# Performance work log

Measured on AMD Instinct MI355X. Metric: run time of the kernel, lower is better.

## Reference

```python
import jax, jax.numpy as jnp
import numpy as np

N_NODES = 100000
N_EDGES = 1600000
D = 128


def setup_inputs() -> dict:
    key = jax.random.key(0)
    k1, k2, k3, k4, k5 = jax.random.split(key, 5)
    scale = 1.0 / np.sqrt(D)
    return {
        "x": jax.random.normal(k1, (N_NODES, D), dtype=jnp.float32),
        "edge_index": jax.random.randint(k2, (2, N_EDGES), 0, N_NODES, dtype=jnp.int64),
        "edge_attr": jax.random.normal(k3, (N_EDGES, D), dtype=jnp.float32),
        "w1": jax.random.normal(k4, (D, D), dtype=jnp.float32) * scale,
        "b1": jnp.zeros((D,), dtype=jnp.float32),
        "w2": jax.random.normal(k5, (D, D), dtype=jnp.float32) * scale,
        "b2": jnp.zeros((D,), dtype=jnp.float32),
    }


def reference(x, edge_index, edge_attr, w1, b1, w2, b2):
    # GINEConv: out = MLP((1+eps)*x + sum_{j->i} ReLU(x_j + e_ij)), eps=0
    src = edge_index[0]  # source node j per edge
    dst = edge_index[1]  # target node i per edge
    msg = jax.nn.relu(x[src] + edge_attr)            # [E, D] edge-wise gather + relu
    agg = jax.ops.segment_sum(msg, dst, num_segments=N_NODES)  # [N, D] scatter-sum
    h = x + agg                                      # (1 + eps)*x with eps = 0
    h = jax.nn.relu(h @ w1 + b1)                     # Linear -> ReLU
    return h @ w2 + b2                               # Linear
```

## Files before the change

### kernel.cpp

```cpp
#include <hip/hip_runtime.h>
#include <stdint.h>

#define N_NODES 100000
#define N_EDGES 1600000
#define D 128
#define ROWS_PAD 100096

typedef long long i64;
typedef __attribute__((ext_vector_type(8))) short bf16x8;
typedef __attribute__((ext_vector_type(4))) float f32x4;
typedef __attribute__((ext_vector_type(4))) float fv4;
typedef __attribute__((ext_vector_type(4))) unsigned short usv4;
typedef __attribute__((ext_vector_type(8))) unsigned short usv8;

__device__ __forceinline__ unsigned short f2bf(float f) {
    union { float f; unsigned u; } v; v.f = f;
    unsigned r = v.u + 0x7fff + ((v.u >> 16) & 1);
    return (unsigned short)(r >> 16);
}
__device__ __forceinline__ float bf2f(unsigned short h) {
    union { unsigned u; float f; } v; v.u = ((unsigned)h) << 16;
    return v.f;
}

__global__ __launch_bounds__(256) void xcvt_kernel(
    const float* __restrict__ x, unsigned short* __restrict__ xb)
{
    const i64 b = ((i64)blockIdx.x * 256 + threadIdx.x) * 8;
    if (b < (i64)N_NODES * D) {
        const fv4 u0 = *reinterpret_cast<const fv4*>(x + b);
        const fv4 u1 = *reinterpret_cast<const fv4*>(x + b + 4);
        usv8 o;
        o.s0 = f2bf(u0.x); o.s1 = f2bf(u0.y); o.s2 = f2bf(u0.z); o.s3 = f2bf(u0.w);
        o.s4 = f2bf(u1.x); o.s5 = f2bf(u1.y); o.s6 = f2bf(u1.z); o.s7 = f2bf(u1.w);
        *reinterpret_cast<usv8*>(xb + b) = o;
    }
}

#define SCAN_CHUNK 1024
#define SCAN_THREADS 256
#define N_CHUNKS ((N_NODES + SCAN_CHUNK - 1) / SCAN_CHUNK)

__global__ __launch_bounds__(256) void count_zero_kernel(int* __restrict__ counts)
{
    const int i = blockIdx.x * 256 + threadIdx.x;
    if (i < N_NODES) counts[i] = 0;
}

__global__ __launch_bounds__(256) void hist_kernel(
    const int* __restrict__ dst, int* __restrict__ counts)
{
    const int e = blockIdx.x * 256 + threadIdx.x;
    if (e < N_EDGES) atomicAdd(&counts[dst[e]], 1);
}

__global__ __launch_bounds__(SCAN_THREADS) void scan_pass1(
    const int* __restrict__ counts, int* __restrict__ blockSums)
{
    __shared__ int sdata[SCAN_THREADS];
    const int b = blockIdx.x, t = threadIdx.x;
    const int base = b * SCAN_CHUNK + t * 4;
    int s = 0;
    #pragma unroll
    for (int k = 0; k < 4; ++k) {
        const int i = base + k;
        if (i < N_NODES) s += counts[i];
    }
    sdata[t] = s; __syncthreads();
    for (int off = SCAN_THREADS / 2; off > 0; off >>= 1) {
        if (t < off) sdata[t] += sdata[t + off];
        __syncthreads();
    }
    if (t == 0) blockSums[b] = sdata[0];
}

__global__ __launch_bounds__(128) void scan_pass2(
    int* __restrict__ blockSums, int* __restrict__ offsets)
{
    __shared__ int sh[128];
    const int t = threadIdx.x;
    const int v = (t < N_CHUNKS) ? blockSums[t] : 0;
    sh[t] = v; __syncthreads();
    for (int off = 1; off < 128; off <<= 1) {
        const int add = (t >= off) ? sh[t - off] : 0;
        __syncthreads();
        sh[t] += add;
        __syncthreads();
    }
    const int incl = sh[t];
    if (t < N_CHUNKS) blockSums[t] = incl - v;
    if (t == N_CHUNKS - 1) offsets[N_NODES] = incl;
}

__global__ __launch_bounds__(SCAN_THREADS) void scan_pass3(
    const int* __restrict__ counts, const int* __restrict__ blockSums,
    int* __restrict__ offsets, int* __restrict__ cursor)
{
    __shared__ int sh[SCAN_THREADS];
    const int b = blockIdx.x, t = threadIdx.x;
    const int base = b * SCAN_CHUNK + t * 4;
    int v[4]; int s = 0;
    #pragma unroll
    for (int k = 0; k < 4; ++k) {
        const int i = base + k;
        v[k] = (i < N_NODES) ? counts[i] : 0;
        s += v[k];
    }
    sh[t] = s; __syncthreads();
    for (int off = 1; off < SCAN_THREADS; off <<= 1) {
        const int add = (t >= off) ? sh[t - off] : 0;
        __syncthreads();
        sh[t] += add;
        __syncthreads();
    }
    int run = blockSums[b] + (sh[t] - s);
    #pragma unroll
    for (int k = 0; k < 4; ++k) {
        const int i = base + k;
        if (i < N_NODES) { offsets[i] = run; cursor[i] = run; }
        run += v[k];
    }
}

__global__ __launch_bounds__(256) void fill_kernel(
    const int* __restrict__ dst, int* __restrict__ cursor, int* __restrict__ bucket)
{
    const int e = blockIdx.x * 256 + threadIdx.x;
    if (e < N_EDGES) {
        const int pos = atomicAdd(&cursor[dst[e]], 1);
        bucket[pos] = e;
    }
}

__global__ __launch_bounds__(256) void pad_zero_kernel(
    unsigned short* __restrict__ h0, unsigned short* __restrict__ h1)
{
    const int i = blockIdx.x * 256 + threadIdx.x;
    const int PADE = (ROWS_PAD - N_NODES) * D;
    if (i < PADE) {
        h0[(i64)N_NODES * D + i] = 0;
        h1[(i64)N_NODES * D + i] = 0;
    }
}

#define PAIR(p) {                                                               \
    const int idx = 2*(p) + half;                                               \
    const bool v = idx < n;                                                     \
    int e_ = __shfl(key, idx);                                                  \
    int s_ = __shfl(sk, idx);                                                   \
    e_ = v ? e_ : 0; s_ = v ? s_ : 0;                                           \
    const usv4 xv = *reinterpret_cast<const usv4*>(xb + (i64)s_ * D + c4);      \
    const fv4 ev = __builtin_nontemporal_load(                                  \
        reinterpret_cast<const fv4*>(ea + (i64)e_ * D + c4));                   \
    if (v) {                                                                    \
        acc.x += fmaxf(bf2f(xv.x) + ev.x, 0.f);                                 \
        acc.y += fmaxf(bf2f(xv.y) + ev.y, 0.f);                                 \
        acc.z += fmaxf(bf2f(xv.z) + ev.z, 0.f);                                 \
        acc.w += fmaxf(bf2f(xv.w) + ev.w, 0.f);                                 \
    }                                                                           \
}

__global__ __launch_bounds__(256) void gather_kernel(
    const float* __restrict__ x,
    const unsigned short* __restrict__ xb,
    const int*   __restrict__ srcIdx,
    const float* __restrict__ ea,
    const int*   __restrict__ offsets,
    const int*   __restrict__ bucket,
    unsigned short* __restrict__ h0)
{
    const int wave = threadIdx.x >> 6;
    const int lane = threadIdx.x & 63;
    const int node = blockIdx.x * 4 + wave;
    if (node >= N_NODES) return;
    const int half = lane >> 5;
    const int c4   = (lane & 31) * 4;

    const int p0 = offsets[node];
    const int p1 = offsets[node + 1];

    fv4 acc;
    if (half == 0) acc = *reinterpret_cast<const fv4*>(x + (i64)node * D + c4);
    else           acc = (fv4){0.f, 0.f, 0.f, 0.f};

    for (int base = p0; base < p1; base += 64) {
        const int n = min(64, p1 - base);

        int key = 0x7fffffff;
        if (lane < n) key = bucket[base + lane];

        #pragma unroll
        for (int k = 2; k <= 64; k <<= 1) {
            #pragma unroll
            for (int j = k >> 1; j > 0; j >>= 1) {
                const int other = __shfl_xor(key, j);
                const bool up    = ((lane & k) == 0);
                const bool lower = ((lane & j) == 0);
                key = (lower == up) ? min(key, other) : max(key, other);
            }
        }

        int sk = 0;
        if (lane < n) sk = srcIdx[key];

        const int npair = (n + 1) >> 1;
        int it = 0;
        for (; it + 3 < npair; it += 4) {
            PAIR(it) PAIR(it + 1) PAIR(it + 2) PAIR(it + 3)
        }
        for (; it < npair; ++it) { PAIR(it) }
    }

    acc.x += __shfl_xor(acc.x, 32);
    acc.y += __shfl_xor(acc.y, 32);
    acc.z += __shfl_xor(acc.z, 32);
    acc.w += __shfl_xor(acc.w, 32);

    if (half == 0) {
        usv4 o;
        o.x = f2bf(acc.x); o.y = f2bf(acc.y);
        o.z = f2bf(acc.z); o.w = f2bf(acc.w);
        *reinterpret_cast<usv4*>(h0 + (i64)node * D + c4) = o;
    }
}

__global__ __launch_bounds__(256) void mlp1_mfma_kernel(
    const unsigned short* __restrict__ hin,
    const float* __restrict__ w,
    const float* __restrict__ bias,
    unsigned short* __restrict__ hout)
{
    const int tid  = threadIdx.x;
    const int wave = tid >> 6;
    const int lane = tid & 63;
    const int g    = lane >> 4;
    const int lr   = lane & 15;
    const int colbase = wave * 32;

    bf16x8 bfrag[4][2];
    #pragma unroll
    for (int ks = 0; ks < 4; ++ks) {
        #pragma unroll
        for (int nt = 0; nt < 2; ++nt) {
            const int col = colbase + nt * 16 + lr;
            const int k0  = ks * 32 + g * 8;
            bf16x8 f;
            #pragma unroll
            for (int j = 0; j < 8; ++j)
                f[j] = (short)f2bf(w[(k0 + j) * D + col]);
            bfrag[ks][nt] = f;
        }
    }
    const float bc0 = bias[colbase + lr];
    const float bc1 = bias[colbase + 16 + lr];

    const int rowbase0 = blockIdx.x * 128;
    #pragma unroll 1
    for (int sub = 0; sub < 8; ++sub) {
        const int rowbase = rowbase0 + sub * 16;
        const int arow = rowbase + lr;

        bf16x8 afrag[4];
        #pragma unroll
        for (int ks = 0; ks < 4; ++ks)
            afrag[ks] = *reinterpret_cast<const bf16x8*>(
                hin + (i64)arow * D + ks * 32 + g * 8);

        f32x4 acc0 = { bc0, bc0, bc0, bc0 };
        f32x4 acc1 = { bc1, bc1, bc1, bc1 };
        #pragma unroll
        for (int ks = 0; ks < 4; ++ks) {
            acc0 = __builtin_amdgcn_mfma_f32_16x16x32_bf16(afrag[ks], bfrag[ks][0], acc0, 0, 0, 0);
            acc1 = __builtin_amdgcn_mfma_f32_16x16x32_bf16(afrag[ks], bfrag[ks][1], acc1, 0, 0, 0);
        }

        #pragma unroll
        for (int r = 0; r < 4; ++r) {
            const int orow = rowbase + g * 4 + r;
            hout[(i64)orow * D + colbase + lr]      = f2bf(fmaxf(acc0[r], 0.f));
            hout[(i64)orow * D + colbase + 16 + lr] = f2bf(fmaxf(acc1[r], 0.f));
        }
    }
}

__global__ __launch_bounds__(256) void mlp2_mfma_kernel(
    const unsigned short* __restrict__ hin,
    const float* __restrict__ w,
    const float* __restrict__ bias,
    float* __restrict__ hout)
{
    const int tid  = threadIdx.x;
    const int wave = tid >> 6;
    const int lane = tid & 63;
    const int g    = lane >> 4;
    const int lr   = lane & 15;
    const int colbase = wave * 32;

    bf16x8 bfrag[4][2];
    #pragma unroll
    for (int ks = 0; ks < 4; ++ks) {
        #pragma unroll
        for (int nt = 0; nt < 2; ++nt) {
            const int col = colbase + nt * 16 + lr;
            const int k0  = ks * 32 + g * 8;
            bf16x8 f;
            #pragma unroll
            for (int j = 0; j < 8; ++j)
                f[j] = (short)f2bf(w[(k0 + j) * D + col]);
            bfrag[ks][nt] = f;
        }
    }
    const float bc0 = bias[colbase + lr];
    const float bc1 = bias[colbase + 16 + lr];

    const int rowbase0 = blockIdx.x * 128;
    #pragma unroll 1
    for (int sub = 0; sub < 8; ++sub) {
        const int rowbase = rowbase0 + sub * 16;
        const int arow = rowbase + lr;

        bf16x8 afrag[4];
        #pragma unroll
        for (int ks = 0; ks < 4; ++ks)
            afrag[ks] = *reinterpret_cast<const bf16x8*>(
                hin + (i64)arow * D + ks * 32 + g * 8);

        f32x4 acc0 = { bc0, bc0, bc0, bc0 };
        f32x4 acc1 = { bc1, bc1, bc1, bc1 };
        #pragma unroll
        for (int ks = 0; ks < 4; ++ks) {
            acc0 = __builtin_amdgcn_mfma_f32_16x16x32_bf16(afrag[ks], bfrag[ks][0], acc0, 0, 0, 0);
            acc1 = __builtin_amdgcn_mfma_f32_16x16x32_bf16(afrag[ks], bfrag[ks][1], acc1, 0, 0, 0);
        }

        #pragma unroll
        for (int r = 0; r < 4; ++r) {
            const int orow = rowbase + g * 4 + r;
            if (orow < N_NODES) {
                hout[(i64)orow * D + colbase + lr]      = acc0[r];
                hout[(i64)orow * D + colbase + 16 + lr] = acc1[r];
            }
        }
    }
}

__global__ __launch_bounds__(256) void init_acc_kernel(
    const float* __restrict__ x, float* __restrict__ acc)
{
    const int i = blockIdx.x * blockDim.x + threadIdx.x;
    const int n = N_NODES * D / 4;
    if (i < n)
        reinterpret_cast<float4*>(acc)[i] = reinterpret_cast<const float4*>(x)[i];
}

__global__ __launch_bounds__(256) void edge_scatter_kernel(
    const float* __restrict__ x,
    const int*  __restrict__ src,
    const int*  __restrict__ dst,
    const float* __restrict__ ea,
    float* __restrict__ acc)
{
    const int lane = threadIdx.x & 31;
    const int grp  = threadIdx.x >> 5;
    const i64 e = (i64)blockIdx.x * 8 + grp;
    if (e >= N_EDGES) return;
    const int s = src[e];
    const int d = dst[e];
    const int j = lane * 4;
    const float4 xv = *reinterpret_cast<const float4*>(x  + (i64)s * D + j);
    const float4 ev = *reinterpret_cast<const float4*>(ea + e * D + j);
    float4 m;
    m.x = fmaxf(xv.x + ev.x, 0.0f);
    m.y = fmaxf(xv.y + ev.y, 0.0f);
    m.z = fmaxf(xv.z + ev.z, 0.0f);
    m.w = fmaxf(xv.w + ev.w, 0.0f);
    float* pp = acc + (i64)d * D + j;
    atomicAdd(pp + 0, m.x);
    atomicAdd(pp + 1, m.y);
    atomicAdd(pp + 2, m.z);
    atomicAdd(pp + 3, m.w);
}

#define MLP_THREADS 512
#define ROWS_PER_CHUNK 16
#define CHUNKS_PER_BLOCK 4
#define ROWS_PER_BLOCK (ROWS_PER_CHUNK * CHUNKS_PER_BLOCK)

template<bool RELU>
__global__ __launch_bounds__(MLP_THREADS) void mlp_layer_kernel(
    const float* __restrict__ hin,
    const float* __restrict__ w,
    const float* __restrict__ b,
    float* __restrict__ hout)
{
    __shared__ float ws_[D * D];
    __shared__ float bs_[D];
    __shared__ float hrow[ROWS_PER_CHUNK][D];

    const int tid = threadIdx.x;
    for (int t = tid; t < D * D / 4; t += MLP_THREADS)
        reinterpret_cast<float4*>(ws_)[t] = reinterpret_cast<const float4*>(w)[t];
    if (tid < D) bs_[tid] = b[tid];

    const int j = tid & (D - 1);
    const int q = tid >> 7;
    const int rowBase = blockIdx.x * ROWS_PER_BLOCK;

    for (int c = 0; c < CHUNKS_PER_BLOCK; ++c) {
        const int chunkRow = rowBase + c * ROWS_PER_CHUNK;
        __syncthreads();
        {
            const int r   = tid >> 5;
            const int col = (tid & 31) * 4;
            const int gi  = chunkRow + r;
            float4 v = make_float4(0.f, 0.f, 0.f, 0.f);
            if (gi < N_NODES)
                v = *reinterpret_cast<const float4*>(hin + (i64)gi * D + col);
            *reinterpret_cast<float4*>(&hrow[r][col]) = v;
        }
        __syncthreads();

        float acc0 = bs_[j], acc1 = bs_[j], acc2 = bs_[j], acc3 = bs_[j];
        const int r0 = q * 4;
        #pragma unroll 4
        for (int k = 0; k < D; ++k) {
            const float wv = ws_[k * D + j];
            acc0 = fmaf(hrow[r0 + 0][k], wv, acc0);
            acc1 = fmaf(hrow[r0 + 1][k], wv, acc1);
            acc2 = fmaf(hrow[r0 + 2][k], wv, acc2);
            acc3 = fmaf(hrow[r0 + 3][k], wv, acc3);
        }
        if (RELU) {
            acc0 = fmaxf(acc0, 0.f); acc1 = fmaxf(acc1, 0.f);
            acc2 = fmaxf(acc2, 0.f); acc3 = fmaxf(acc3, 0.f);
        }
        const int gi = chunkRow + r0;
        if (gi + 0 < N_NODES) hout[(i64)(gi + 0) * D + j] = acc0;
        if (gi + 1 < N_NODES) hout[(i64)(gi + 1) * D + j] = acc1;
        if (gi + 2 < N_NODES) hout[(i64)(gi + 2) * D + j] = acc2;
        if (gi + 3 < N_NODES) hout[(i64)(gi + 3) * D + j] = acc3;
    }
}

extern "C" void kernel_launch(void* const* d_in, const int* in_sizes, int n_in,
                              void* d_out, int out_size, void* d_ws, size_t ws_size,
                              hipStream_t stream)
{
    const float* x  = (const float*)d_in[0];
    const int*   ei = (const int*)  d_in[1];
    const float* ea = (const float*)d_in[2];
    const float* w1 = (const float*)d_in[3];
    const float* b1 = (const float*)d_in[4];
    const float* w2 = (const float*)d_in[5];
    const float* b2 = (const float*)d_in[6];
    float* out = (float*)d_out;

    const int* src = ei;
    const int* dst = ei + N_EDGES;

    const size_t INT_REGION = (size_t)N_NODES + (N_NODES + 1) + N_NODES + 128 + N_EDGES;
    const size_t X_ELEMS    = (size_t)N_NODES * D;
    const size_t H_ELEMS    = (size_t)ROWS_PAD * D;
    const size_t WS_NEEDED  = INT_REGION * 4 + 64 + (X_ELEMS + 2 * H_ELEMS) * 2;

    if (ws_size >= WS_NEEDED) {
        int* counts    = (int*)d_ws;
        int* offsets   = counts + N_NODES;
        int* cursor    = offsets + (N_NODES + 1);
        int* blockSums = cursor + N_NODES;
        int* bucket    = blockSums + 128;
        uintptr_t p = (uintptr_t)(bucket + N_EDGES);
        p = (p + 63) & ~(uintptr_t)63;
        unsigned short* xb = (unsigned short*)p;
        unsigned short* h0 = xb + X_ELEMS;
        unsigned short* h1 = h0 + H_ELEMS;

        xcvt_kernel<<<(int)(X_ELEMS / 8 + 255) / 256, 256, 0, stream>>>(x, xb);
        count_zero_kernel<<<(N_NODES + 255) / 256, 256, 0, stream>>>(counts);
        hist_kernel<<<(N_EDGES + 255) / 256, 256, 0, stream>>>(dst, counts);
        scan_pass1<<<N_CHUNKS, SCAN_THREADS, 0, stream>>>(counts, blockSums);
        scan_pass2<<<1, 128, 0, stream>>>(blockSums, offsets);
        scan_pass3<<<N_CHUNKS, SCAN_THREADS, 0, stream>>>(counts, blockSums, offsets, cursor);
        fill_kernel<<<(N_EDGES + 255) / 256, 256, 0, stream>>>(dst, cursor, bucket);
        pad_zero_kernel<<<48, 256, 0, stream>>>(h0, h1);
        gather_kernel<<<(N_NODES + 3) / 4, 256, 0, stream>>>(x, xb, src, ea, offsets, bucket, h0);

        const int mlpBlocks = ROWS_PAD / 128;
        mlp1_mfma_kernel<<<mlpBlocks, 256, 0, stream>>>(h0, w1, b1, h1);
        mlp2_mfma_kernel<<<mlpBlocks, 256, 0, stream>>>(h1, w2, b2, out);
    } else {
        const int n = N_NODES * D / 4;
        init_acc_kernel<<<(n + 255) / 256, 256, 0, stream>>>(x, out);
        edge_scatter_kernel<<<(N_EDGES + 7) / 8, 256, 0, stream>>>(x, src, dst, ea, out);
        const int blocks = (N_NODES + ROWS_PER_BLOCK - 1) / ROWS_PER_BLOCK;
        mlp_layer_kernel<true ><<<blocks, MLP_THREADS, 0, stream>>>(out, w1, b1, out);
        mlp_layer_kernel<false><<<blocks, MLP_THREADS, 0, stream>>>(out, w2, b2, out);
    }
}
```

Measured before the change: 486.7 us.

## Fuse MLP layers via LDS, pack src into bucket, merge prep kernels

Fuses the two MLP MFMA kernels into one that keeps the hidden layer in shared memory rather than writing and rereading it from global memory. The fill kernel now stores (edge, src) pairs so the gather kernel no longer does a dependent srcIdx lookup; both values are carried through the bitonic sort. The bf16 conversion, count zeroing and pad zeroing are merged into one prep kernel, which removes launches. The self term now comes from the bf16 copy of x instead of fp32 x, which slightly lowers precision.

```diff
diff --git a/kernel.cpp b/kernel.cpp
--- a/kernel.cpp
+++ b/kernel.cpp
@@ -23,10 +23,12 @@
     return v.f;
 }
 
-__global__ __launch_bounds__(256) void xcvt_kernel(
-    const float* __restrict__ x, unsigned short* __restrict__ xb)
-{
-    const i64 b = ((i64)blockIdx.x * 256 + threadIdx.x) * 8;
+__global__ __launch_bounds__(256) void prep_kernel(
+    const float* __restrict__ x, unsigned short* __restrict__ xb,
+    int* __restrict__ counts, unsigned short* __restrict__ h0)
+{
+    const int i = blockIdx.x * 256 + threadIdx.x;
+    const i64 b = (i64)i * 8;
     if (b < (i64)N_NODES * D) {
         const fv4 u0 = *reinterpret_cast<const fv4*>(x + b);
         const fv4 u1 = *reinterpret_cast<const fv4*>(x + b + 4);
@@ -35,17 +37,14 @@
         o.s4 = f2bf(u1.x); o.s5 = f2bf(u1.y); o.s6 = f2bf(u1.z); o.s7 = f2bf(u1.w);
         *reinterpret_cast<usv8*>(xb + b) = o;
     }
+    if (i < N_NODES) counts[i] = 0;
+    if (i < (ROWS_PAD - N_NODES) * D)
+        h0[(i64)N_NODES * D + i] = 0;
 }
 
 #define SCAN_CHUNK 1024
 #define SCAN_THREADS 256
 #define N_CHUNKS ((N_NODES + SCAN_CHUNK - 1) / SCAN_CHUNK)
-
-__global__ __launch_bounds__(256) void count_zero_kernel(int* __restrict__ counts)
-{
-    const int i = blockIdx.x * 256 + threadIdx.x;
-    if (i < N_NODES) counts[i] = 0;
-}
 
 __global__ __launch_bounds__(256) void hist_kernel(
     const int* __restrict__ dst, int* __restrict__ counts)
@@ -122,24 +121,14 @@
     }
 }
 
-__global__ __launch_bounds__(256) void fill_kernel(
-    const int* __restrict__ dst, int* __restrict__ cursor, int* __restrict__ bucket)
+__global__ __launch_bounds__(256) void fill2_kernel(
+    const int* __restrict__ src, const int* __restrict__ dst,
+    int* __restrict__ cursor, int2* __restrict__ bucket2)
 {
     const int e = blockIdx.x * 256 + threadIdx.x;
     if (e < N_EDGES) {
         const int pos = atomicAdd(&cursor[dst[e]], 1);
-        bucket[pos] = e;
-    }
-}
-
-__global__ __launch_bounds__(256) void pad_zero_kernel(
-    unsigned short* __restrict__ h0, unsigned short* __restrict__ h1)
-{
-    const int i = blockIdx.x * 256 + threadIdx.x;
-    const int PADE = (ROWS_PAD - N_NODES) * D;
-    if (i < PADE) {
-        h0[(i64)N_NODES * D + i] = 0;
-        h1[(i64)N_NODES * D + i] = 0;
+        bucket2[pos] = make_int2(e, src[e]);
     }
 }
 
@@ -147,7 +136,7 @@
     const int idx = 2*(p) + half;                                               \
     const bool v = idx < n;                                                     \
     int e_ = __shfl(key, idx);                                                  \
-    int s_ = __shfl(sk, idx);                                                   \
+    int s_ = __shfl(sv, idx);                                                   \
     e_ = v ? e_ : 0; s_ = v ? s_ : 0;                                           \
     const usv4 xv = *reinterpret_cast<const usv4*>(xb + (i64)s_ * D + c4);      \
     const fv4 ev = __builtin_nontemporal_load(                                  \
@@ -161,12 +150,10 @@
 }
 
 __global__ __launch_bounds__(256) void gather_kernel(
-    const float* __restrict__ x,
     const unsigned short* __restrict__ xb,
-    const int*   __restrict__ srcIdx,
     const float* __restrict__ ea,
-    const int*   __restrict__ offsets,
-    const int*   __restrict__ bucket,
+    const int*  __restrict__ offsets,
+    const int2* __restrict__ bucket2,
     unsigned short* __restrict__ h0)
 {
     const int wave = threadIdx.x >> 6;
@@ -179,29 +166,34 @@
     const int p0 = offsets[node];
     const int p1 = offsets[node + 1];
 
-    fv4 acc;
-    if (half == 0) acc = *reinterpret_cast<const fv4*>(x + (i64)node * D + c4);
-    else           acc = (fv4){0.f, 0.f, 0.f, 0.f};
+    fv4 acc = (fv4){0.f, 0.f, 0.f, 0.f};
+    if (half == 0) {
+        const usv4 xv = *reinterpret_cast<const usv4*>(xb + (i64)node * D + c4);
+        acc.x = bf2f(xv.x); acc.y = bf2f(xv.y);
+        acc.z = bf2f(xv.z); acc.w = bf2f(xv.w);
+    }
 
     for (int base = p0; base < p1; base += 64) {
         const int n = min(64, p1 - base);
 
-        int key = 0x7fffffff;
-        if (lane < n) key = bucket[base + lane];
+        int key = 0x7fffffff, sv = 0;
+        if (lane < n) {
+            const int2 t = bucket2[base + lane];
+            key = t.x; sv = t.y;
+        }
 
         #pragma unroll
         for (int k = 2; k <= 64; k <<= 1) {
             #pragma unroll
             for (int j = k >> 1; j > 0; j >>= 1) {
-                const int other = __shfl_xor(key, j);
+                const int ok = __shfl_xor(key, j);
+                const int os = __shfl_xor(sv, j);
                 const bool up    = ((lane & k) == 0);
                 const bool lower = ((lane & j) == 0);
-                key = (lower == up) ? min(key, other) : max(key, other);
+                const bool take  = (lower == up) ? (ok < key) : (ok > key);
+                if (take) { key = ok; sv = os; }
             }
         }
-
-        int sk = 0;
-        if (lane < n) sk = srcIdx[key];
 
         const int npair = (n + 1) >> 1;
         int it = 0;
@@ -224,18 +216,21 @@
     }
 }
 
-__global__ __launch_bounds__(256) void mlp1_mfma_kernel(
+__global__ __launch_bounds__(256) void mlp_fused_kernel(
     const unsigned short* __restrict__ hin,
-    const float* __restrict__ w,
-    const float* __restrict__ bias,
-    unsigned short* __restrict__ hout)
-{
+    const float* __restrict__ w1, const float* __restrict__ b1,
+    const float* __restrict__ w2, const float* __restrict__ b2,
+    float* __restrict__ out)
+{
+    __shared__ unsigned short h1[128][136];
+
     const int tid  = threadIdx.x;
     const int wave = tid >> 6;
     const int lane = tid & 63;
     const int g    = lane >> 4;
     const int lr   = lane & 15;
     const int colbase = wave * 32;
+    const int rowbase0 = blockIdx.x * 128;
 
     bf16x8 bfrag[4][2];
     #pragma unroll
@@ -247,18 +242,16 @@
             bf16x8 f;
             #pragma unroll
             for (int j = 0; j < 8; ++j)
-                f[j] = (short)f2bf(w[(k0 + j) * D + col]);
+                f[j] = (short)f2bf(w1[(k0 + j) * D + col]);
             bfrag[ks][nt] = f;
         }
     }
-    const float bc0 = bias[colbase + lr];
-    const float bc1 = bias[colbase + 16 + lr];
-
-    const int rowbase0 = blockIdx.x * 128;
+    float bc0 = b1[colbase + lr];
+    float bc1 = b1[colbase + 16 + lr];
+
     #pragma unroll 1
     for (int sub = 0; sub < 8; ++sub) {
-        const int rowbase = rowbase0 + sub * 16;
-        const int arow = rowbase + lr;
+        const int arow = rowbase0 + sub * 16 + lr;
 
         bf16x8 afrag[4];
         #pragma unroll
@@ -276,27 +269,14 @@
 
         #pragma unroll
         for (int r = 0; r < 4; ++r) {
-            const int orow = rowbase + g * 4 + r;
-            hout[(i64)orow * D + colbase + lr]      = f2bf(fmaxf(acc0[r], 0.f));
-            hout[(i64)orow * D + colbase + 16 + lr] = f2bf(fmaxf(acc1[r], 0.f));
-        }
-    }
-}
-
-__global__ __launch_bounds__(256) void mlp2_mfma_kernel(
-    const unsigned short* __restrict__ hin,
-    const float* __restrict__ w,
-    const float* __restrict__ bias,
-    float* __restrict__ hout)
-{
-    const int tid  = threadIdx.x;
-    const int wave = tid >> 6;
-    const int lane = tid & 63;
-    const int g    = lane >> 4;
-    const int lr   = lane & 15;
-    const int colbase = wave * 32;
-
-    bf16x8 bfrag[4][2];
+            const int rl = sub * 16 + g * 4 + r;
+            h1[rl][colbase + lr]      = f2bf(fmaxf(acc0[r], 0.f));
+            h1[rl][colbase + 16 + lr] = f2bf(fmaxf(acc1[r], 0.f));
+        }
+    }
+
+    __syncthreads();
+
     #pragma unroll
     for (int ks = 0; ks < 4; ++ks) {
         #pragma unroll
@@ -306,24 +286,21 @@
             bf16x8 f;
             #pragma unroll
             for (int j = 0; j < 8; ++j)
-                f[j] = (short)f2bf(w[(k0 + j) * D + col]);
+                f[j] = (short)f2bf(w2[(k0 + j) * D + col]);
             bfrag[ks][nt] = f;
         }
     }
-    const float bc0 = bias[colbase + lr];
-    const float bc1 = bias[colbase + 16 + lr];
-
-    const int rowbase0 = blockIdx.x * 128;
+    bc0 = b2[colbase + lr];
+    bc1 = b2[colbase + 16 + lr];
+
     #pragma unroll 1
     for (int sub = 0; sub < 8; ++sub) {
-        const int rowbase = rowbase0 + sub * 16;
-        const int arow = rowbase + lr;
+        const int rl = sub * 16 + lr;
 
         bf16x8 afrag[4];
         #pragma unroll
         for (int ks = 0; ks < 4; ++ks)
-            afrag[ks] = *reinterpret_cast<const bf16x8*>(
-                hin + (i64)arow * D + ks * 32 + g * 8);
+            afrag[ks] = *reinterpret_cast<const bf16x8*>(&h1[rl][ks * 32 + g * 8]);
 
         f32x4 acc0 = { bc0, bc0, bc0, bc0 };
         f32x4 acc1 = { bc1, bc1, bc1, bc1 };
@@ -335,10 +312,10 @@
 
         #pragma unroll
         for (int r = 0; r < 4; ++r) {
-            const int orow = rowbase + g * 4 + r;
+            const int orow = rowbase0 + sub * 16 + g * 4 + r;
             if (orow < N_NODES) {
-                hout[(i64)orow * D + colbase + lr]      = acc0[r];
-                hout[(i64)orow * D + colbase + 16 + lr] = acc1[r];
+                out[(i64)orow * D + colbase + lr]      = acc0[r];
+                out[(i64)orow * D + colbase + 16 + lr] = acc1[r];
             }
         }
     }
@@ -458,36 +435,33 @@
     const int* src = ei;
     const int* dst = ei + N_EDGES;
 
-    const size_t INT_REGION = (size_t)N_NODES + (N_NODES + 1) + N_NODES + 128 + N_EDGES;
+    const size_t INT_REGION = (size_t)N_NODES + (N_NODES + 1) + N_NODES + 128;
     const size_t X_ELEMS    = (size_t)N_NODES * D;
     const size_t H_ELEMS    = (size_t)ROWS_PAD * D;
-    const size_t WS_NEEDED  = INT_REGION * 4 + 64 + (X_ELEMS + 2 * H_ELEMS) * 2;
+    const size_t WS_NEEDED  = INT_REGION * 4 + 64 + (size_t)N_EDGES * 8 + 64
+                            + (X_ELEMS + H_ELEMS) * 2;
 
     if (ws_size >= WS_NEEDED) {
         int* counts    = (int*)d_ws;
         int* offsets   = counts + N_NODES;
         int* cursor    = offsets + (N_NODES + 1);
         int* blockSums = cursor + N_NODES;
-        int* bucket    = blockSums + 128;
-        uintptr_t p = (uintptr_t)(bucket + N_EDGES);
+        uintptr_t p = (uintptr_t)(blockSums + 128);
+        p = (p + 63) & ~(uintptr_t)63;
+        int2* bucket2 = (int2*)p;
+        p = (uintptr_t)(bucket2 + N_EDGES);
         p = (p + 63) & ~(uintptr_t)63;
         unsigned short* xb = (unsigned short*)p;
         unsigned short* h0 = xb + X_ELEMS;
-        unsigned short* h1 = h0 + H_ELEMS;
-
-        xcvt_kernel<<<(int)(X_ELEMS / 8 + 255) / 256, 256, 0, stream>>>(x, xb);
-        count_zero_kernel<<<(N_NODES + 255) / 256, 256, 0, stream>>>(counts);
+
+        prep_kernel<<<(int)(X_ELEMS / 8 + 255) / 256, 256, 0, stream>>>(x, xb, counts, h0);
         hist_kernel<<<(N_EDGES + 255) / 256, 256, 0, stream>>>(dst, counts);
         scan_pass1<<<N_CHUNKS, SCAN_THREADS, 0, stream>>>(counts, blockSums);
         scan_pass2<<<1, 128, 0, stream>>>(blockSums, offsets);
         scan_pass3<<<N_CHUNKS, SCAN_THREADS, 0, stream>>>(counts, blockSums, offsets, cursor);
-        fill_kernel<<<(N_EDGES + 255) / 256, 256, 0, stream>>>(dst, cursor, bucket);
-        pad_zero_kernel<<<48, 256, 0, stream>>>(h0, h1);
-        gather_kernel<<<(N_NODES + 3) / 4, 256, 0, stream>>>(x, xb, src, ea, offsets, bucket, h0);
-
-        const int mlpBlocks = ROWS_PAD / 128;
-        mlp1_mfma_kernel<<<mlpBlocks, 256, 0, stream>>>(h0, w1, b1, h1);
-        mlp2_mfma_kernel<<<mlpBlocks, 256, 0, stream>>>(h1, w2, b2, out);
+        fill2_kernel<<<(N_EDGES + 255) / 256, 256, 0, stream>>>(src, dst, cursor, bucket2);
+        gather_kernel<<<(N_NODES + 3) / 4, 256, 0, stream>>>(xb, ea, offsets, bucket2, h0);
+        mlp_fused_kernel<<<ROWS_PAD / 128, 256, 0, stream>>>(h0, w1, b1, w2, b2, out);
     } else {
         const int n = N_NODES * D / 4;
         init_acc_kernel<<<(n + 255) / 256, 256, 0, stream>>>(x, out);
```

Result: faster. 437.5 us (-10.1%).
